# Kernel tuning notes

Hardware: AMD Instinct MI355X
Metric: run time of the kernel (lower is better)

The kernel has to match this reference:

```python
import jax, jax.numpy as jnp
import numpy as np
from jax import lax

H, W = 32, 32
HEADS = 8
EPS_LN = 1e-5


def layer_norm(x, g, b):
    mu = jnp.mean(x, axis=-1, keepdims=True)
    var = jnp.mean((x - mu) ** 2, axis=-1, keepdims=True)
    return (x - mu) * lax.rsqrt(var + EPS_LN) * g + b


def l2norm(x):  # F.normalize along last dim, eps=1e-12
    n = jnp.sqrt(jnp.sum(x * x, axis=-1, keepdims=True))
    return x / jnp.maximum(n, 1e-12)


def channel_attention(x, qkv_w, temp, proj_w, proj_b):
    B, N, C = x.shape
    d = C // HEADS
    qkv = (x @ qkv_w).reshape(B, N, 3, HEADS, d).transpose(2, 0, 3, 1, 4)  # [3,B,h,N,d]
    q, k, v = qkv[0], qkv[1], qkv[2]
    q = l2norm(q.swapaxes(-2, -1))  # [B,h,d,N], normalized over N
    k = l2norm(k.swapaxes(-2, -1))
    v = v.swapaxes(-2, -1)          # [B,h,d,N]
    attn = jnp.einsum('bhdn,bhen->bhde', q, k) * temp  # [B,h,d,d]
    attn = jax.nn.softmax(attn, axis=-1)
    out = jnp.einsum('bhde,bhen->bhdn', attn, v)       # [B,h,d,N]
    out = out.transpose(0, 3, 1, 2).reshape(B, N, C)
    return out @ proj_w + proj_b


def cross_attention(x1, x2, rp_w, rp_b, cn_g, cn_b):
    # head_count = 1 (efficient/linear attention)
    B, N, D = x1.shape
    keys = x2.swapaxes(1, 2)            # [B,D,N]
    values = x1.swapaxes(1, 2)          # [B,D,N]
    key = jax.nn.softmax(keys, axis=2)  # softmax over tokens
    query = jax.nn.softmax(keys, axis=1)  # softmax over channels
    context = jnp.einsum('bdn,ben->bde', key, values)     # [B,Dk,Dv]
    attended = jnp.einsum('bde,bdn->ben', context, query)  # [B,Dv,N]
    agg = attended.reshape(B, D, H, W)
    # 1x1 conv reprojection D -> 2D
    rep = jnp.einsum('bdhw,ed->behw', agg, rp_w) + rp_b[None, :, None, None]
    rep = rep.reshape(B, 2 * D, N).transpose(0, 2, 1)     # [B,N,2D]
    return layer_norm(rep, cn_g, cn_b)


def mix_ffn(x, fc1_w, fc1_b, dw_w, dw_b, fc2_w, fc2_b):
    B, N, _ = x.shape
    c2 = fc1_w.shape[1]
    h1 = x @ fc1_w + fc1_b                                 # [B,N,c2]
    t = h1.swapaxes(1, 2).reshape(B, c2, H, W)
    conv = lax.conv_general_dilated(
        t, dw_w, window_strides=(1, 1), padding='SAME',
        feature_group_count=c2,
        dimension_numbers=('NCHW', 'OIHW', 'NCHW')) + dw_b[None, :, None, None]
    h2 = conv.reshape(B, c2, N).swapaxes(1, 2)             # [B,N,c2]
    return jax.nn.gelu(h2, approximate=False) @ fc2_w + fc2_b


def reference(x1, x2, ln1_g, ln1_b, ca_qkv_w, ca_temp, ca_proj_w, ca_proj_b,
              ln3_g, ln3_b, rp_w, rp_b, cn_g, cn_b, ln2_g, ln2_b,
              fc1_w, fc1_b, dw_w, dw_b, fc2_w, fc2_b):
    # NOTE: original code uses norm1 + channel_attn1 on BOTH streams
    channel1 = x1 + channel_attention(layer_norm(x1, ln1_g, ln1_b), ca_qkv_w, ca_temp, ca_proj_w, ca_proj_b)
    channel2 = x2 + channel_attention(layer_norm(x2, ln1_g, ln1_b), ca_qkv_w, ca_temp, ca_proj_w, ca_proj_b)
    n1 = layer_norm(channel1, ln3_g, ln3_b)
    n2 = layer_norm(channel2, ln3_g, ln3_b)
    attn = cross_attention(n1, n2, rp_w, rp_b, cn_g, cn_b)
    tx = jnp.concatenate([channel1, channel2], axis=2) + attn  # [B,N,2D]
    mx = tx + mix_ffn(layer_norm(tx, ln2_g, ln2_b), fc1_w, fc1_b, dw_w, dw_b, fc2_w, fc2_b)
    return mx


def setup_inputs() -> dict:
    key = jax.random.key(0)
    ks = jax.random.split(key, 8)
    B, N, D = 16, 1024, 384
    s = 0.02
    return {
        'x1': jax.random.normal(ks[0], (B, N, D), jnp.float32),
        'x2': jax.random.normal(ks[1], (B, N, D), jnp.float32),
        'ln1_g': jnp.ones((D,), jnp.float32), 'ln1_b': jnp.zeros((D,), jnp.float32),
        'ca_qkv_w': jax.random.normal(ks[2], (D, 3 * D), jnp.float32) * s,
        'ca_temp': jnp.ones((HEADS, 1, 1), jnp.float32),
        'ca_proj_w': jax.random.normal(ks[3], (D, D), jnp.float32) * s,
        'ca_proj_b': jnp.zeros((D,), jnp.float32),
        'ln3_g': jnp.ones((D,), jnp.float32), 'ln3_b': jnp.zeros((D,), jnp.float32),
        'rp_w': jax.random.normal(ks[4], (2 * D, D), jnp.float32) * s,
        'rp_b': jnp.zeros((2 * D,), jnp.float32),
        'cn_g': jnp.ones((2 * D,), jnp.float32), 'cn_b': jnp.zeros((2 * D,), jnp.float32),
        'ln2_g': jnp.ones((2 * D,), jnp.float32), 'ln2_b': jnp.zeros((2 * D,), jnp.float32),
        'fc1_w': jax.random.normal(ks[5], (2 * D, 4 * D), jnp.float32) * s,
        'fc1_b': jnp.zeros((4 * D,), jnp.float32),
        'dw_w': jax.random.normal(ks[6], (4 * D, 1, 3, 3), jnp.float32) * s,
        'dw_b': jnp.zeros((4 * D,), jnp.float32),
        'fc2_w': jax.random.normal(ks[7], (4 * D, 2 * D), jnp.float32) * s,
        'fc2_b': jnp.zeros((2 * D,), jnp.float32),
    }
```

## Files before the change

### kernel.cpp

```cpp
#include <hip/hip_runtime.h>
#include <math.h>

#define BN 16
#define NN 1024
#define DD 384
#define D2 768
#define C2 1536
#define NHEAD 8
#define DH 48

#define SZ_ND   (BN*NN*DD)
#define SZ_N2D  (BN*NN*D2)
#define SZ_NC2  (BN*NN*C2)
#define M2      32768
#define MH      16384

typedef __bf16 bf16x8 __attribute__((ext_vector_type(8)));
typedef float f32x4v __attribute__((ext_vector_type(4)));
typedef unsigned short u16x4 __attribute__((ext_vector_type(4)));

__device__ __forceinline__ unsigned short f2bf(float x){
  unsigned int u = __float_as_uint(x);
  u += 0x7FFFu + ((u >> 16) & 1u);
  return (unsigned short)(u >> 16);
}
__device__ __forceinline__ float bf2f(unsigned short h){
  return __uint_as_float(((unsigned int)h) << 16);
}

__device__ __forceinline__ float blockReduceSum256(float v){
  __shared__ float red[4];
  #pragma unroll
  for (int o=32;o;o>>=1) v += __shfl_down(v,o,64);
  if ((threadIdx.x&63)==0) red[threadIdx.x>>6]=v;
  __syncthreads();
  float r = red[0]+red[1]+red[2]+red[3];
  __syncthreads();
  return r;
}
__device__ __forceinline__ float blockReduceMax256(float v){
  __shared__ float red[4];
  #pragma unroll
  for (int o=32;o;o>>=1) v = fmaxf(v, __shfl_down(v,o,64));
  if ((threadIdx.x&63)==0) red[threadIdx.x>>6]=v;
  __syncthreads();
  float r = fmaxf(fmaxf(red[0],red[1]),fmaxf(red[2],red[3]));
  __syncthreads();
  return r;
}

__global__ __launch_bounds__(256) void ln_kernel(const float* __restrict__ in,
    const float* __restrict__ g, const float* __restrict__ b,
    float* __restrict__ out, int C){
  const int row = blockIdx.x;
  const float* x = in + (size_t)row*C;
  float s=0.f;
  for (int i=threadIdx.x;i<C;i+=256) s += x[i];
  s = blockReduceSum256(s);
  const float mu = s / (float)C;
  float v=0.f;
  for (int i=threadIdx.x;i<C;i+=256){ float d = x[i]-mu; v += d*d; }
  v = blockReduceSum256(v);
  const float rs = rsqrtf(v/(float)C + 1e-5f);
  float* o = out + (size_t)row*C;
  for (int i=threadIdx.x;i<C;i+=256) o[i] = (x[i]-mu)*rs*g[i] + b[i];
}

__global__ __launch_bounds__(256) void ln_split2_kernel(const float* __restrict__ in1,
    const float* __restrict__ in2, int Mh,
    const float* __restrict__ g, const float* __restrict__ b,
    unsigned short* __restrict__ oh, unsigned short* __restrict__ ol, int C){
  const int row = blockIdx.x;
  const float* x = (row < Mh) ? (in1 + (size_t)row*C) : (in2 + (size_t)(row-Mh)*C);
  float s=0.f;
  for (int i=threadIdx.x;i<C;i+=256) s += x[i];
  s = blockReduceSum256(s);
  const float mu = s / (float)C;
  float v=0.f;
  for (int i=threadIdx.x;i<C;i+=256){ float d = x[i]-mu; v += d*d; }
  v = blockReduceSum256(v);
  const float rs = rsqrtf(v/(float)C + 1e-5f);
  unsigned short* ohp = oh + (size_t)row*C;
  unsigned short* olp = ol + (size_t)row*C;
  for (int i=threadIdx.x;i<C;i+=256){
    float val = (x[i]-mu)*rs*g[i] + b[i];
    unsigned short hh = f2bf(val);
    ohp[i] = hh; olp[i] = f2bf(val - bf2f(hh));
  }
}

__global__ __launch_bounds__(256) void rowsoftmax_split_kernel(const float* __restrict__ in,
    unsigned short* __restrict__ oh, unsigned short* __restrict__ ol, int C){
  const int row = blockIdx.x;
  const float* x = in + (size_t)row*C;
  float m = -3.0e38f;
  for (int i=threadIdx.x;i<C;i+=256) m = fmaxf(m, x[i]);
  m = blockReduceMax256(m);
  float s = 0.f;
  for (int i=threadIdx.x;i<C;i+=256) s += expf(x[i]-m);
  s = blockReduceSum256(s);
  const float inv = 1.f/s;
  unsigned short* ohp = oh + (size_t)row*C;
  unsigned short* olp = ol + (size_t)row*C;
  for (int i=threadIdx.x;i<C;i+=256){
    float p = expf(x[i]-m)*inv;
    unsigned short hh = f2bf(p);
    ohp[i] = hh; olp[i] = f2bf(p - bf2f(hh));
  }
}

__global__ __launch_bounds__(256) void colsoftmax_tsplit_kernel(const float* __restrict__ in,
    unsigned short* __restrict__ oh, unsigned short* __restrict__ ol){
  __shared__ float tile[64][33];
  __shared__ unsigned short outh[32][66], outl[32][66];
  __shared__ float redm[8][32], reds[8][32];
  const int d0 = blockIdx.x*32, b = blockIdx.y;
  const int t = threadIdx.x, dl = t & 31, nc = t >> 5;
  const float* p = in + (size_t)b*NN*DD + d0;

  float m_run = -3.0e38f, s_run = 0.f;
  for (int tb = 0; tb < 16; tb++){
    const int n0 = tb*64;
    #pragma unroll
    for (int k=0;k<8;k++){
      int e = t + k*256;
      int row = e >> 5, col = e & 31;
      tile[row][col] = p[(size_t)(n0+row)*DD + col];
    }
    __syncthreads();
    float lm = -3.0e38f;
    #pragma unroll
    for (int r=0;r<8;r++) lm = fmaxf(lm, tile[nc*8+r][dl]);
    redm[nc][dl] = lm;
    __syncthreads();
    float tm = redm[0][dl];
    #pragma unroll
    for (int q=1;q<8;q++) tm = fmaxf(tm, redm[q][dl]);
    float m_new = fmaxf(m_run, tm);
    float ls = 0.f;
    #pragma unroll
    for (int r=0;r<8;r++) ls += expf(tile[nc*8+r][dl] - m_new);
    reds[nc][dl] = ls;
    __syncthreads();
    float ts = reds[0][dl];
    #pragma unroll
    for (int q=1;q<8;q++) ts += reds[q][dl];
    s_run = s_run * expf(m_run - m_new) + ts;
    m_run = m_new;
    __syncthreads();
  }

  const float inv = 1.f / s_run, mm = m_run;
  unsigned short* qh = oh + ((size_t)b*DD + d0)*NN;
  unsigned short* ql = ol + ((size_t)b*DD + d0)*NN;
  for (int tb = 0; tb < 16; tb++){
    const int n0 = tb*64;
    #pragma unroll
    for (int k=0;k<8;k++){
      int e = t + k*256;
      int row = e >> 5, col = e & 31;
      tile[row][col] = p[(size_t)(n0+row)*DD + col];
    }
    __syncthreads();
    #pragma unroll
    for (int r=0;r<8;r++){
      int row = nc*8 + r;
      float val = expf(tile[row][dl] - mm) * inv;
      unsigned short hh = f2bf(val);
      outh[dl][row] = hh;
      outl[dl][row] = f2bf(val - bf2f(hh));
    }
    __syncthreads();
    #pragma unroll
    for (int k=0;k<8;k++){
      int e = t + k*256;
      int dd = e >> 6, nn = e & 63;
      qh[(size_t)dd*NN + n0 + nn] = outh[dd][nn];
      ql[(size_t)dd*NN + n0 + nn] = outl[dd][nn];
    }
    __syncthreads();
  }
}

__global__ __launch_bounds__(256) void tsplit_kernel(const float* __restrict__ in,
    unsigned short* __restrict__ oh, unsigned short* __restrict__ ol, int R, int Cc){
  const size_t zb = (size_t)blockIdx.z * R * Cc;
  const float* ip = in + zb;
  unsigned short* ohp = oh + zb;
  unsigned short* olp = ol + zb;
  __shared__ float tile[32][33];
  const int c0 = blockIdx.x*32, r0 = blockIdx.y*32;
  const int j = threadIdx.x & 31, i4 = threadIdx.x >> 5;
  #pragma unroll
  for (int s=0;s<4;s++){
    int i = i4*4+s;
    tile[i][j] = ip[(size_t)(r0+i)*Cc + c0 + j];
  }
  __syncthreads();
  #pragma unroll
  for (int s=0;s<4;s++){
    int i = i4*4+s;
    float x = tile[j][i];
    unsigned short h = f2bf(x);
    ohp[(size_t)(c0+i)*R + r0 + j] = h;
    olp[(size_t)(c0+i)*R + r0 + j] = f2bf(x - bf2f(h));
  }
}

__global__ __launch_bounds__(256) void chattn_mfma_kernel(
    const unsigned int* __restrict__ qp, const float* __restrict__ temp,
    unsigned short* __restrict__ coh, unsigned short* __restrict__ col)
{
  const int bh = blockIdx.x, b = bh >> 3, h = bh & 7;
  const int t = threadIdx.x, w = t >> 6, lane = t & 63;
  const int lr = lane & 15, g = lane >> 4;

  __shared__ __align__(16) unsigned char ldsA[27648];
  unsigned short (*Qh)[72] = (unsigned short(*)[72])(ldsA);
  unsigned short (*Ql)[72] = (unsigned short(*)[72])(ldsA + 6912);
  unsigned short (*Kh)[72] = (unsigned short(*)[72])(ldsA + 13824);
  unsigned short (*Kl)[72] = (unsigned short(*)[72])(ldsA + 20736);
  unsigned short (*Vh)[72] = (unsigned short(*)[72])(ldsA);
  unsigned short (*Vl)[72] = (unsigned short(*)[72])(ldsA + 9216);
  __shared__ unsigned short Ph[48][72], Pl[48][72];
  __shared__ float S[48][49];
  __shared__ float qn[48], kn[48];

  const size_t base = (size_t)b*NN*1152 + (size_t)h*48;

  int agrp[3], apr[3], aoff[3];
  #pragma unroll
  for (int l=0;l<3;l++){
    int idx = l*256+t;
    int mo = (idx>=384) ? 1 : 0;
    int a = idx - mo*384;
    agrp[l] = a%12; apr[l] = a/12; aoff[l] = mo*384;
  }

  f32x4v acc[12];
  #pragma unroll
  for (int i=0;i<12;i++) acc[i] = (f32x4v){0.f,0.f,0.f,0.f};

  uint4 p0[3], p1[3];
  #pragma unroll
  for (int l=0;l<3;l++){
    const size_t a = base + (size_t)(apr[l]*2)*1152 + aoff[l] + agrp[l]*4;
    p0[l] = *(const uint4*)(qp + a);
    p1[l] = *(const uint4*)(qp + a + 1152);
  }

  for (int nc=0; nc<16; nc++){
    #pragma unroll
    for (int l=0;l<3;l++){
      unsigned short (*Dh)[72] = aoff[l] ? Kh : Qh;
      unsigned short (*Dl)[72] = aoff[l] ? Kl : Ql;
      const unsigned w0[4] = {p0[l].x, p0[l].y, p0[l].z, p0[l].w};
      const unsigned w1[4] = {p1[l].x, p1[l].y, p1[l].z, p1[l].w};
      #pragma unroll
      for (int c=0;c<4;c++){
        int d = agrp[l]*4+c;
        *(unsigned int*)&Dh[d][apr[l]*2] = (w0[c] & 0xffffu) | (w1[c] << 16);
        *(unsigned int*)&Dl[d][apr[l]*2] = (w0[c] >> 16)     | (w1[c] & 0xffff0000u);
      }
    }
    __syncthreads();
    if (nc < 15){
      #pragma unroll
      for (int l=0;l<3;l++){
        const size_t a = base + (size_t)((nc+1)*64 + apr[l]*2)*1152 + aoff[l] + agrp[l]*4;
        p0[l] = *(const uint4*)(qp + a);
        p1[l] = *(const uint4*)(qp + a + 1152);
      }
    }
    if (w < 3){
      #pragma unroll
      for (int ks=0;ks<2;ks++){
        bf16x8 a_h = *(const bf16x8*)&Qh[w*16+lr][ks*32+g*8];
        bf16x8 a_l = *(const bf16x8*)&Ql[w*16+lr][ks*32+g*8];
        #pragma unroll
        for (int c=0;c<3;c++){
          bf16x8 b_h = *(const bf16x8*)&Kh[c*16+lr][ks*32+g*8];
          bf16x8 b_l = *(const bf16x8*)&Kl[c*16+lr][ks*32+g*8];
          acc[c] = __builtin_amdgcn_mfma_f32_16x16x32_bf16(a_h, b_h, acc[c], 0,0,0);
          acc[c] = __builtin_amdgcn_mfma_f32_16x16x32_bf16(a_l, b_h, acc[c], 0,0,0);
          acc[c] = __builtin_amdgcn_mfma_f32_16x16x32_bf16(a_h, b_l, acc[c], 0,0,0);
        }
      }
    } else {
      #pragma unroll
      for (int ks=0;ks<2;ks++){
        #pragma unroll
        for (int c=0;c<3;c++){
          bf16x8 qh_ = *(const bf16x8*)&Qh[c*16+lr][ks*32+g*8];
          bf16x8 ql_ = *(const bf16x8*)&Ql[c*16+lr][ks*32+g*8];
          bf16x8 kh_ = *(const bf16x8*)&Kh[c*16+lr][ks*32+g*8];
          bf16x8 kl_ = *(const bf16x8*)&Kl[c*16+lr][ks*32+g*8];
          acc[c]   = __builtin_amdgcn_mfma_f32_16x16x32_bf16(qh_, qh_, acc[c],   0,0,0);
          acc[3+c] = __builtin_amdgcn_mfma_f32_16x16x32_bf16(qh_, ql_, acc[3+c], 0,0,0);
          acc[6+c] = __builtin_amdgcn_mfma_f32_16x16x32_bf16(kh_, kh_, acc[6+c], 0,0,0);
          acc[9+c] = __builtin_amdgcn_mfma_f32_16x16x32_bf16(kh_, kl_, acc[9+c], 0,0,0);
        }
      }
    }
    __syncthreads();
  }

  const float tp = temp[h];
  if (w == 3){
    if ((lane>>4) == ((lane&15)>>2)){
      int p = lane & 15, r = p & 3;
      #pragma unroll
      for (int c=0;c<3;c++){
        float q2 = fmaxf(acc[c][r]   + 2.f*acc[3+c][r], 0.f);
        float k2 = fmaxf(acc[6+c][r] + 2.f*acc[9+c][r], 0.f);
        qn[c*16+p] = fmaxf(sqrtf(q2), 1e-12f);
        kn[c*16+p] = fmaxf(sqrtf(k2), 1e-12f);
      }
    }
  }
  __syncthreads();
  if (w < 3){
    #pragma unroll
    for (int c=0;c<3;c++){
      #pragma unroll
      for (int r=0;r<4;r++){
        int i = w*16 + g*4 + r, j = c*16 + lr;
        S[i][j] = acc[c][r]*tp/(qn[i]*kn[j]);
      }
    }
  }
  __syncthreads();

  int vgrp[3], vtk[3];
  #pragma unroll
  for (int l=0;l<3;l++){ int idx=l*256+t; vtk[l]=idx/12; vgrp[l]=idx%12; }
  uint4 pv[3];
  #pragma unroll
  for (int l=0;l<3;l++){
    const size_t a = base + (size_t)vtk[l]*1152 + 768 + vgrp[l]*4;
    pv[l] = *(const uint4*)(qp + a);
  }

  if (t < 48){
    float m = -3.0e38f;
    for (int j=0;j<48;j++) m = fmaxf(m, S[t][j]);
    float s = 0.f;
    for (int j=0;j<48;j++){ float e_ = expf(S[t][j]-m); S[t][j] = e_; s += e_; }
    float inv = 1.f/s;
    for (int j=0;j<48;j++){
      float p = S[t][j]*inv;
      unsigned short hp = f2bf(p);
      Ph[t][j] = hp; Pl[t][j] = f2bf(p - bf2f(hp));
    }
    #pragma unroll
    for (int j=48;j<64;j++){ Ph[t][j]=0; Pl[t][j]=0; }
  } else {
    const u16x4 z4 = (u16x4){0,0,0,0};
    for (int idx=t-48; idx<512; idx+=208){
      int tk = idx>>3, q = idx&7;
      if (q<4) *(u16x4*)&Vh[tk][48+(q&3)*4] = z4;
      else     *(u16x4*)&Vl[tk][48+(q&3)*4] = z4;
    }
  }
  __syncthreads();

  bf16x8 pfh[3][2], pfl[3][2];
  #pragma unroll
  for (int it=0;it<3;it++)
    #pragma unroll
    for (int ks=0;ks<2;ks++){
      pfh[it][ks] = *(const bf16x8*)&Ph[it*16+lr][ks*32+g*8];
      pfl[it][ks] = *(const bf16x8*)&Pl[it*16+lr][ks*32+g*8];
    }

  for (int vc=0; vc<16; vc++){
    #pragma unroll
    for (int l=0;l<3;l++){
      const unsigned pw[4] = {pv[l].x, pv[l].y, pv[l].z, pv[l].w};
      u16x4 hv, lv;
      #pragma unroll
      for (int c=0;c<4;c++){
        hv[c] = (unsigned short)(pw[c] & 0xffffu);
        lv[c] = (unsigned short)(pw[c] >> 16);
      }
      *(u16x4*)&Vh[vtk[l]][vgrp[l]*4] = hv;
      *(u16x4*)&Vl[vtk[l]][vgrp[l]*4] = lv;
    }
    __syncthreads();
    if (vc < 15){
      #pragma unroll
      for (int l=0;l<3;l++){
        const size_t a = base + (size_t)((vc+1)*64+vtk[l])*1152 + 768 + vgrp[l]*4;
        pv[l] = *(const uint4*)(qp + a);
      }
    }
    bf16x8 vfh[2], vfl[2];
    #pragma unroll
    for (int ks=0;ks<2;ks++){
      vfh[ks] = *(const bf16x8*)&Vh[w*16+lr][ks*32+g*8];
      vfl[ks] = *(const bf16x8*)&Vl[w*16+lr][ks*32+g*8];
    }
    f32x4v o[3];
    #pragma unroll
    for (int it=0;it<3;it++) o[it] = (f32x4v){0.f,0.f,0.f,0.f};
    #pragma unroll
    for (int it=0;it<3;it++)
      #pragma unroll
      for (int ks=0;ks<2;ks++){
        o[it] = __builtin_amdgcn_mfma_f32_16x16x32_bf16(pfh[it][ks], vfh[ks], o[it], 0,0,0);
        o[it] = __builtin_amdgcn_mfma_f32_16x16x32_bf16(pfl[it][ks], vfh[ks], o[it], 0,0,0);
        o[it] = __builtin_amdgcn_mfma_f32_16x16x32_bf16(pfh[it][ks], vfl[ks], o[it], 0,0,0);
      }
    const int n = vc*64 + w*16 + lr;
    #pragma unroll
    for (int it=0;it<3;it++){
      const size_t off = ((size_t)b*NN + n)*DD + h*48 + it*16 + g*4;
      u16x4 hv, lv;
      #pragma unroll
      for (int r=0;r<4;r++){
        float x = o[it][r];
        unsigned short hh = f2bf(x);
        hv[r] = hh; lv[r] = f2bf(x - bf2f(hh));
      }
      *(u16x4*)(coh + off) = hv;
      *(u16x4*)(col + off) = lv;
    }
    __syncthreads();
  }
}

__global__ __launch_bounds__(256) void wprep2_kernel(
    const float* __restrict__ qkvw, unsigned short* __restrict__ qwh, unsigned short* __restrict__ qwl,
    const float* __restrict__ projw, unsigned short* __restrict__ pwh, unsigned short* __restrict__ pwl)
{
  __shared__ float tile[32][33];
  const int bid = blockIdx.x;
  const float* in; unsigned short *oh, *ol; int Nin, bx, by;
  if (bid < 432){ in = qkvw;  oh = qwh; ol = qwl; Nin = 1152; bx = bid % 36; by = bid / 36; }
  else { int k = bid - 432; in = projw; oh = pwh; ol = pwl; Nin = DD;   bx = k % 12;  by = k / 12; }
  const int n0 = bx*32, k0 = by*32;
  const int j = threadIdx.x & 31, i4 = threadIdx.x >> 5;
  #pragma unroll
  for (int s=0;s<4;s++){
    int i = i4*4+s;
    tile[i][j] = in[(size_t)(k0+i)*Nin + n0 + j];
  }
  __syncthreads();
  #pragma unroll
  for (int s=0;s<4;s++){
    int i = i4*4+s;
    float x = tile[j][i];
    unsigned short h = f2bf(x);
    oh[(size_t)(n0+i)*DD + k0 + j] = h;
    ol[(size_t)(n0+i)*DD + k0 + j] = f2bf(x - bf2f(h));
  }
}

__global__ __launch_bounds__(256) void wconv_t_kernel(const float* __restrict__ in,
    unsigned short* __restrict__ oh, unsigned short* __restrict__ ol, int K, int Nin){
  __shared__ float tile[32][33];
  const int n0 = blockIdx.x*32, k0 = blockIdx.y*32;
  const int j = threadIdx.x & 31, i4 = threadIdx.x >> 5;
  #pragma unroll
  for (int s=0;s<4;s++){
    int i = i4*4+s;
    tile[i][j] = (n0 + j < Nin) ? in[(size_t)(k0+i)*Nin + n0 + j] : 0.f;
  }
  __syncthreads();
  #pragma unroll
  for (int s=0;s<4;s++){
    int i = i4*4+s;
    float x = tile[j][i];
    unsigned short h = f2bf(x);
    oh[(size_t)(n0+i)*K + k0 + j] = h;
    ol[(size_t)(n0+i)*K + k0 + j] = f2bf(x - bf2f(h));
  }
}

__global__ __launch_bounds__(256) void wconv_kernel(const float* __restrict__ in,
    unsigned short* __restrict__ oh, unsigned short* __restrict__ ol, int n){
  int i = blockIdx.x*256 + threadIdx.x;
  if (i < n){
    float x = in[i];
    unsigned short h = f2bf(x);
    oh[i] = h;
    ol[i] = f2bf(x - bf2f(h));
  }
}

template<bool BIAS_, bool RES_, bool SPLIT_, bool PACK32_>
__global__ __launch_bounds__(256) void gemm_bf16x3s_kernel(
    const unsigned short* __restrict__ Ah, const unsigned short* __restrict__ Al,
    const unsigned short* __restrict__ Bh, const unsigned short* __restrict__ Bl,
    const float* __restrict__ bias, const float* __restrict__ res,
    const float* __restrict__ res2, int Mh2,
    float* __restrict__ C, unsigned short* __restrict__ Ch, unsigned short* __restrict__ Cl,
    int M, int N, int K, size_t sAz, size_t sBz, size_t sCz)
{
  const int t = threadIdx.x;
  const int nwg = gridDim.x*gridDim.y;
  const int lin = blockIdx.y*gridDim.x + blockIdx.x;
  const int swz = ((nwg & 7)==0) ? ((lin & 7)*(nwg >> 3) + (lin >> 3)) : lin;
  const int bx = swz % gridDim.x, by = swz / gridDim.x;
  const int m0 = by*128, n0 = bx*128;
  const size_t zo = (size_t)blockIdx.z;

  __shared__ unsigned short As_h0[128][32], As_l0[128][32];
  __shared__ unsigned short Bs_h0[128][32], Bs_l0[128][32];
  __shared__ unsigned short As_h1[128][32], As_l1[128][32];
  __shared__ unsigned short Bs_h1[128][32], Bs_l1[128][32];

  const unsigned short* Ahb = Ah + zo*sAz + (size_t)m0*K;
  const unsigned short* Alb = Al + zo*sAz + (size_t)m0*K;
  const unsigned short* Bhb = Bh + zo*sBz + (size_t)n0*K;
  const unsigned short* Blb = Bl + zo*sBz + (size_t)n0*K;

  f32x4v acc[4][4];
  #pragma unroll
  for (int i=0;i<4;i++)
    #pragma unroll
    for (int j=0;j<4;j++) acc[i][j] = (f32x4v){0.f,0.f,0.f,0.f};

  const int w  = t >> 6;
  const int wm = w >> 1, wn = w & 1;
  const int lr = t & 15, g = (t & 63) >> 4;
  const int srow = t >> 1;
  const int kb0  = (t & 1)*2;
  const int ssw  = (srow >> 1) & 3;
  const int ks0  = ((kb0+0) ^ ssw)*8;
  const int ks1  = ((kb0+1) ^ ssw)*8;

  uint4 aAh0,aAh1,aAl0,aAl1,aBh0,aBh1,aBl0,aBl1;
  uint4 bAh0,bAh1,bAl0,bAl1,bBh0,bBh1,bBl0,bBl1;

#define LOADT(P, K0) { \
    const size_t go0 = (size_t)srow*K + (size_t)(K0) + (size_t)(kb0*8); \
    P##Ah0 = *(const uint4*)(Ahb + go0); P##Ah1 = *(const uint4*)(Ahb + go0 + 8); \
    P##Al0 = *(const uint4*)(Alb + go0); P##Al1 = *(const uint4*)(Alb + go0 + 8); \
    P##Bh0 = *(const uint4*)(Bhb + go0); P##Bh1 = *(const uint4*)(Bhb + go0 + 8); \
    P##Bl0 = *(const uint4*)(Blb + go0); P##Bl1 = *(const uint4*)(Blb + go0 + 8); }

#define WRITET(BUF, P) { \
    *(uint4*)&As_h##BUF[srow][ks0] = P##Ah0; *(uint4*)&As_h##BUF[srow][ks1] = P##Ah1; \
    *(uint4*)&As_l##BUF[srow][ks0] = P##Al0; *(uint4*)&As_l##BUF[srow][ks1] = P##Al1; \
    *(uint4*)&Bs_h##BUF[srow][ks0] = P##Bh0; *(uint4*)&Bs_h##BUF[srow][ks1] = P##Bh1; \
    *(uint4*)&Bs_l##BUF[srow][ks0] = P##Bl0; *(uint4*)&Bs_l##BUF[srow][ks1] = P##Bl1; }

#define COMPUTET(BUF) { \
    bf16x8 ah[4], al[4], bhf[4], blf[4]; \
    _Pragma("unroll") \
    for (int i=0;i<4;i++){ \
      const int ra = wm*64 + i*16 + lr; \
      const int ka = (g ^ ((ra>>1)&3))*8; \
      ah[i]  = *(const bf16x8*)&As_h##BUF[ra][ka]; \
      al[i]  = *(const bf16x8*)&As_l##BUF[ra][ka]; \
      const int rb = wn*64 + i*16 + lr; \
      const int kb = (g ^ ((rb>>1)&3))*8; \
      bhf[i] = *(const bf16x8*)&Bs_h##BUF[rb][kb]; \
      blf[i] = *(const bf16x8*)&Bs_l##BUF[rb][kb]; \
    } \
    _Pragma("unroll") \
    for (int mi=0;mi<4;mi++) \
      _Pragma("unroll") \
      for (int ni=0;ni<4;ni++){ \
        f32x4v c_ = acc[mi][ni]; \
        c_ = __builtin_amdgcn_mfma_f32_16x16x32_bf16(ah[mi], bhf[ni], c_, 0,0,0); \
        c_ = __builtin_amdgcn_mfma_f32_16x16x32_bf16(al[mi], bhf[ni], c_, 0,0,0); \
        c_ = __builtin_amdgcn_mfma_f32_16x16x32_bf16(ah[mi], blf[ni], c_, 0,0,0); \
        acc[mi][ni] = c_; \
      } }

  const int nk = K >> 5;
  LOADT(a, 0);
  WRITET(0, a);
  LOADT(a, 32);
  __syncthreads();

  for (int kt = 0; kt < nk; kt += 2){
    if (kt+2 < nk) LOADT(b, (kt+2)*32);
    COMPUTET(0);
    WRITET(1, a);
    __syncthreads();
    if (kt+3 < nk) LOADT(a, (kt+3)*32);
    COMPUTET(1);
    if (kt+2 < nk){ WRITET(0, b); }
    __syncthreads();
  }

#undef LOADT
#undef WRITET
#undef COMPUTET

  if (PACK32_){
    unsigned int* Cp = (unsigned int*)Ch + zo*sCz;
    #pragma unroll
    for (int ni=0;ni<4;ni++){
      const int col = n0 + wn*64 + ni*16 + lr;
      #pragma unroll
      for (int mi=0;mi<4;mi++){
        const int r0 = m0 + wm*64 + mi*16 + g*4;
        #pragma unroll
        for (int r=0;r<4;r++){
          float v = acc[mi][ni][r];
          unsigned short hv = f2bf(v);
          unsigned short lv = f2bf(v - bf2f(hv));
          Cp[(size_t)(r0+r)*N + col] = (unsigned)hv | ((unsigned)lv << 16);
        }
      }
    }
  } else if (SPLIT_){
    unsigned short* Chb = Ch + zo*sCz;
    unsigned short* Clb = Cl + zo*sCz;
    #pragma unroll
    for (int ni=0;ni<4;ni++){
      const int col = n0 + wn*64 + ni*16 + lr;
      #pragma unroll
      for (int mi=0;mi<4;mi++){
        const int r0 = m0 + wm*64 + mi*16 + g*4;
        #pragma unroll
        for (int r=0;r<4;r++){
          float v = acc[mi][ni][r];
          unsigned short hv = f2bf(v);
          const size_t off = (size_t)(r0+r)*N + col;
          Chb[off] = hv;
          Clb[off] = f2bf(v - bf2f(hv));
        }
      }
    }
  } else {
    float* Cb = C + zo*sCz;
    const float* resb = nullptr;
    size_t roff = 0;
    if (RES_){
      if (res2 != nullptr && m0 >= Mh2){ resb = res2; roff = (size_t)Mh2; }
      else resb = res + zo*sCz;
    }
    #pragma unroll
    for (int ni=0;ni<4;ni++){
      const int col = n0 + wn*64 + ni*16 + lr;
      const float bb = BIAS_ ? bias[col] : 0.f;
      #pragma unroll
      for (int mi=0;mi<4;mi++){
        const int r0 = m0 + wm*64 + mi*16 + g*4;
        #pragma unroll
        for (int r=0;r<4;r++){
          float v = acc[mi][ni][r] + bb;
          if (RES_) v += resb[((size_t)(r0+r) - roff)*N + col];
          Cb[(size_t)(r0+r)*N + col] = v;
        }
      }
    }
  }
}

__global__ __launch_bounds__(256) void ln_concat_ln2_kernel(const float* __restrict__ rep,
    const float* __restrict__ g1, const float* __restrict__ b1,
    const float* __restrict__ ch1, const float* __restrict__ ch2,
    const float* __restrict__ g2, const float* __restrict__ b2,
    float* __restrict__ tx, unsigned short* __restrict__ y2h, unsigned short* __restrict__ y2l){
  const int row = blockIdx.x;
  const float* x = rep + (size_t)row*D2;
  float xv[3];
  float s=0.f;
  #pragma unroll
  for (int q=0;q<3;q++){ xv[q] = x[threadIdx.x + q*256]; s += xv[q]; }
  s = blockReduceSum256(s);
  const float mu = s / (float)D2;
  float v=0.f;
  #pragma unroll
  for (int q=0;q<3;q++){ float d = xv[q]-mu; v += d*d; }
  v = blockReduceSum256(v);
  const float rs = rsqrtf(v/(float)D2 + 1e-5f);
  float tv[3];
  #pragma unroll
  for (int q=0;q<3;q++){
    int i = threadIdx.x + q*256;
    float val = (xv[q]-mu)*rs*g1[i] + b1[i];
    float rv = (i<DD) ? ch1[(size_t)row*DD + i] : ch2[(size_t)row*DD + i - DD];
    tv[q] = val + rv;
    tx[(size_t)row*D2 + i] = tv[q];
  }
  float s2 = tv[0]+tv[1]+tv[2];
  s2 = blockReduceSum256(s2);
  const float mu2 = s2 / (float)D2;
  float v2=0.f;
  #pragma unroll
  for (int q=0;q<3;q++){ float d = tv[q]-mu2; v2 += d*d; }
  v2 = blockReduceSum256(v2);
  const float rs2 = rsqrtf(v2/(float)D2 + 1e-5f);
  #pragma unroll
  for (int q=0;q<3;q++){
    int i = threadIdx.x + q*256;
    float y = (tv[q]-mu2)*rs2*g2[i] + b2[i];
    unsigned short hh = f2bf(y);
    y2h[(size_t)row*D2 + i] = hh;
    y2l[(size_t)row*D2 + i] = f2bf(y - bf2f(hh));
  }
}

__global__ __launch_bounds__(256) void dwconv_gelu_kernel(const float* __restrict__ h1,
    const float* __restrict__ w, const float* __restrict__ bias,
    unsigned short* __restrict__ gh, unsigned short* __restrict__ gl){
  const int idx = blockIdx.x*256 + threadIdx.x;
  const int b   = idx / 12288;
  const int r   = idx - b*12288;
  const int hh  = r / 384;
  const int c4  = r - hh*384;
  const int c   = c4*4;
  const float* base = h1 + (size_t)b*NN*C2 + c;
  const size_t obase = ((size_t)b*NN + hh*32)*C2 + c;

  f32x4v wk[9];
  #pragma unroll
  for (int k=0;k<9;k++){
    f32x4v t_;
    #pragma unroll
    for (int q=0;q<4;q++) t_[q] = w[(size_t)(c+q)*9 + k];
    wk[k] = t_;
  }
  f32x4v bvv;
  {
    const float4 bb = *(const float4*)(bias + c);
    bvv = (f32x4v){bb.x, bb.y, bb.z, bb.w};
  }

  const bool hm = (hh > 0), hp = (hh < 31);
  const f32x4v z4 = (f32x4v){0.f,0.f,0.f,0.f};
  const size_t rm = (size_t)((hh-1)*32)*C2;
  const size_t r0 = (size_t)( hh   *32)*C2;
  const size_t rp = (size_t)((hh+1)*32)*C2;

  f32x4v A0,A1,A2, B0,B1,B2, C0,C1,C2c;
  A0=z4; A1=z4; A2=z4;
  B0 = hm ? *(const f32x4v*)(base + rm) : z4;
  B1 =      *(const f32x4v*)(base + r0);
  B2 = hp ? *(const f32x4v*)(base + rp) : z4;
  C0 = hm ? *(const f32x4v*)(base + rm + C2) : z4;
  C1 =      *(const f32x4v*)(base + r0 + C2);
  C2c= hp ? *(const f32x4v*)(base + rp + C2) : z4;

  for (int ww=0; ww<32; ww++){
    f32x4v N0,N1,N2;
    if (ww < 30){
      const size_t co_ = (size_t)(ww+2)*C2;
      N0 = hm ? *(const f32x4v*)(base + rm + co_) : z4;
      N1 =      *(const f32x4v*)(base + r0 + co_) ;
      N2 = hp ? *(const f32x4v*)(base + rp + co_) : z4;
    } else { N0=z4; N1=z4; N2=z4; }

    f32x4v s = bvv;
    s += wk[0]*A0 + wk[1]*B0 + wk[2]*C0;
    s += wk[3]*A1 + wk[4]*B1 + wk[5]*C1;
    s += wk[6]*A2 + wk[7]*B2 + wk[8]*C2c;

    u16x4 hv, lv;
    #pragma unroll
    for (int q=0;q<4;q++){
      float rlt = 0.5f*s[q]*(1.f + erff(s[q]*0.70710678118654752f));
      unsigned short hhv = f2bf(rlt);
      hv[q] = hhv; lv[q] = f2bf(rlt - bf2f(hhv));
    }
    *(u16x4*)(gh + obase + (size_t)ww*C2) = hv;
    *(u16x4*)(gl + obase + (size_t)ww*C2) = lv;

    A0=B0; A1=B1; A2=B2;
    B0=C0; B1=C1; B2=C2c;
    C0=N0; C1=N1; C2c=N2;
  }
}

extern "C" void kernel_launch(void* const* d_in, const int* in_sizes, int n_in,
                              void* d_out, int out_size, void* d_ws, size_t ws_size,
                              hipStream_t stream) {
  const float* x1     = (const float*)d_in[0];
  const float* x2     = (const float*)d_in[1];
  const float* ln1_g  = (const float*)d_in[2];
  const float* ln1_b  = (const float*)d_in[3];
  const float* qkv_w  = (const float*)d_in[4];
  const float* ca_temp= (const float*)d_in[5];
  const float* proj_w = (const float*)d_in[6];
  const float* proj_b = (const float*)d_in[7];
  const float* ln3_g  = (const float*)d_in[8];
  const float* ln3_b  = (const float*)d_in[9];
  const float* rp_w   = (const float*)d_in[10];
  const float* rp_b   = (const float*)d_in[11];
  const float* cn_g   = (const float*)d_in[12];
  const float* cn_b   = (const float*)d_in[13];
  const float* ln2_g  = (const float*)d_in[14];
  const float* ln2_b  = (const float*)d_in[15];
  const float* fc1_w  = (const float*)d_in[16];
  const float* fc1_b  = (const float*)d_in[17];
  const float* dw_w   = (const float*)d_in[18];
  const float* dw_b   = (const float*)d_in[19];
  const float* fc2_w  = (const float*)d_in[20];
  const float* fc2_b  = (const float*)d_in[21];
  float* out = (float*)d_out;
  float* W   = (float*)d_ws;

  unsigned short* ycoh = (unsigned short*)out;
  unsigned short* ycol = ycoh + 12582912u;
  unsigned short* coh  = ycoh;
  unsigned short* col  = ycol;
  unsigned int*   qkvp = (unsigned int*)W;
  unsigned short* qkvwT_h  = (unsigned short*)(W + 37748736ull);
  unsigned short* qkvwT_l  = qkvwT_h + 442368u;
  unsigned short* projwT_h = qkvwT_l + 442368u;
  unsigned short* projwT_l = projwT_h + 147456u;
  float* ch12 = W;
  float* n12  = W + 12582912ull;
  unsigned short* QSh = (unsigned short*)(W + 25165824ull);
  unsigned short* QSl = QSh + 6291456u;
  unsigned short* KSt_h = (unsigned short*)(W + 31457280ull);
  unsigned short* KSt_l = KSt_h + 6291456u;
  unsigned short* rpw_h = (unsigned short*)(W + 37748736ull);
  unsigned short* rpw_l = rpw_h + 294912u;
  unsigned short* n1t_h = (unsigned short*)(W + 38043648ull);
  unsigned short* n1t_l = n1t_h + 6291456u;
  unsigned short* ctxT_h = (unsigned short*)(W + 12582912ull);
  unsigned short* ctxT_l = ctxT_h + 2359296u;
  unsigned short* ATbh = (unsigned short*)(W + 14942208ull);
  unsigned short* ATbl = ATbh + 6291456u;
  float* rep = W + 25165824ull;
  float* txp = out;
  unsigned short* y2h = (unsigned short*)(W + 37748736ull);
  unsigned short* y2l = y2h + 12582912u;
  float* h1 = W;
  unsigned short* fc1wT_h = (unsigned short*)(W + 25165824ull);
  unsigned short* fc1wT_l = fc1wT_h + 1179648u;
  unsigned short* gh = (unsigned short*)(W + 25165824ull);
  unsigned short* gl = (unsigned short*)(W + 37748736ull);
  unsigned short* fc2wT_h = (unsigned short*)W;
  unsigned short* fc2wT_l = fc2wT_h + 1179648u;

  wprep2_kernel<<<dim3(576), dim3(256), 0, stream>>>(
      qkv_w, qkvwT_h, qkvwT_l, proj_w, projwT_h, projwT_l);

  ln_split2_kernel<<<dim3(M2), dim3(256), 0, stream>>>(x1, x2, MH, ln1_g, ln1_b, ycoh, ycol, DD);
  gemm_bf16x3s_kernel<false,false,false,true><<<dim3(1152/128, M2/128), dim3(256), 0, stream>>>(
      ycoh, ycol, qkvwT_h, qkvwT_l, nullptr, nullptr, nullptr, 0,
      nullptr, (unsigned short*)qkvp, nullptr, M2, 1152, DD, 0,0,0);
  chattn_mfma_kernel<<<dim3(32*NHEAD), dim3(256), 0, stream>>>(qkvp, ca_temp, coh, col);
  gemm_bf16x3s_kernel<true,true,false,false><<<dim3(DD/128, M2/128), dim3(256), 0, stream>>>(
      coh, col, projwT_h, projwT_l, proj_b, x1, x2, MH,
      ch12, nullptr, nullptr, M2, DD, DD, 0,0,0);

  wconv_kernel<<<dim3(294912/256), dim3(256), 0, stream>>>(rp_w, rpw_h, rpw_l, 294912);
  ln_kernel<<<dim3(M2), dim3(256), 0, stream>>>(ch12, ln3_g, ln3_b, n12, DD);
  const float* n2half = n12 + (size_t)MH*DD;
  rowsoftmax_split_kernel<<<dim3(MH), dim3(256), 0, stream>>>(n2half, QSh, QSl, DD);
  colsoftmax_tsplit_kernel<<<dim3(DD/32, BN), dim3(256), 0, stream>>>(n2half, KSt_h, KSt_l);
  tsplit_kernel<<<dim3(DD/32, NN/32, BN), dim3(256), 0, stream>>>(n12, n1t_h, n1t_l, NN, DD);
  gemm_bf16x3s_kernel<false,false,true,false><<<dim3(DD/128, DD/128, BN), dim3(256), 0, stream>>>(
      n1t_h, n1t_l, KSt_h, KSt_l, nullptr, nullptr, nullptr, 0,
      nullptr, ctxT_h, ctxT_l, DD, DD, NN, (size_t)DD*NN, (size_t)DD*NN, (size_t)DD*DD);
  gemm_bf16x3s_kernel<false,false,true,false><<<dim3(DD/128, NN/128, BN), dim3(256), 0, stream>>>(
      QSh, QSl, ctxT_h, ctxT_l, nullptr, nullptr, nullptr, 0,
      nullptr, ATbh, ATbl, NN, DD, DD, (size_t)NN*DD, (size_t)DD*DD, (size_t)NN*DD);
  gemm_bf16x3s_kernel<true,false,false,false><<<dim3(D2/128, MH/128), dim3(256), 0, stream>>>(
      ATbh, ATbl, rpw_h, rpw_l, rp_b, nullptr, nullptr, 0,
      rep, nullptr, nullptr, MH, D2, DD, 0,0,0);
  ln_concat_ln2_kernel<<<dim3(MH), dim3(256), 0, stream>>>(
      rep, cn_g, cn_b, ch12, ch12 + (size_t)MH*DD, ln2_g, ln2_b, txp, y2h, y2l);

  wconv_t_kernel<<<dim3(C2/32, D2/32), dim3(256), 0, stream>>>(fc1_w, fc1wT_h, fc1wT_l, D2, C2);
  gemm_bf16x3s_kernel<true,false,false,false><<<dim3(C2/128, MH/128), dim3(256), 0, stream>>>(
      y2h, y2l, fc1wT_h, fc1wT_l, fc1_b, nullptr, nullptr, 0,
      h1, nullptr, nullptr, MH, C2, D2, 0,0,0);
  dwconv_gelu_kernel<<<dim3(196608/256), dim3(256), 0, stream>>>(h1, dw_w, dw_b, gh, gl);
  wconv_t_kernel<<<dim3(D2/32, C2/32), dim3(256), 0, stream>>>(fc2_w, fc2wT_h, fc2wT_l, C2, D2);
  gemm_bf16x3s_kernel<true,true,false,false><<<dim3(D2/128, MH/128), dim3(256), 0, stream>>>(
      gh, gl, fc2wT_h, fc2wT_l, fc2_b, txp, nullptr, 0,
      out, nullptr, nullptr, MH, D2, C2, 0,0,0);
}
```

Baseline: 847.8 us.

## Add 256x256-tile 8-wave bf16x3 GEMM with phased prefetch for FFN and reprojection

```diff
diff --git a/kernel.cpp b/kernel.cpp
--- a/kernel.cpp
+++ b/kernel.cpp
@@ -648,6 +648,130 @@
           if (RES_) v += resb[((size_t)(r0+r) - roff)*N + col];
           Cb[(size_t)(r0+r)*N + col] = v;
         }
+      }
+    }
+  }
+}
+
+template<bool BIAS_, bool RES_>
+__global__ __launch_bounds__(512, 2) void gemm_bf16x3_8ph_kernel(
+    const unsigned short* __restrict__ Ah, const unsigned short* __restrict__ Al,
+    const unsigned short* __restrict__ Bh, const unsigned short* __restrict__ Bl,
+    const float* __restrict__ bias, const float* __restrict__ res,
+    float* __restrict__ C, int M, int N, int K)
+{
+  const int t = threadIdx.x;
+  const int nwg = gridDim.x*gridDim.y;
+  const int lin = blockIdx.y*gridDim.x + blockIdx.x;
+  const int swz = ((nwg & 7)==0) ? ((lin & 7)*(nwg >> 3) + (lin >> 3)) : lin;
+  const int bx = swz % gridDim.x, by = swz / gridDim.x;
+  const int m0 = by*256, n0 = bx*256;
+
+  __shared__ unsigned short As_h[2][256][32], As_l[2][256][32];
+  __shared__ unsigned short Bs_h[2][256][32], Bs_l[2][256][32];
+
+  const unsigned short* Ahb = Ah + (size_t)m0*K;
+  const unsigned short* Alb = Al + (size_t)m0*K;
+  const unsigned short* Bhb = Bh + (size_t)n0*K;
+  const unsigned short* Blb = Bl + (size_t)n0*K;
+
+  f32x4v acc[8][4];
+  #pragma unroll
+  for (int i=0;i<8;i++)
+    #pragma unroll
+    for (int j=0;j<4;j++) acc[i][j] = (f32x4v){0.f,0.f,0.f,0.f};
+
+  const int w  = t >> 6;
+  const int wm = w >> 2, wn = w & 3;
+  const int lr = t & 15, g = (t & 63) >> 4;
+  const int srow = t >> 1;
+  const int kb0  = (t & 1)*2;
+  const int ssw  = (srow >> 1) & 3;
+  const int ks0  = ((kb0+0) ^ ssw)*8;
+  const int ks1  = ((kb0+1) ^ ssw)*8;
+
+  uint4 aA0,aA1,aA2,aA3, aB0,aB1,aB2,aB3;
+  uint4 bA0,bA1,bA2,bA3, bB0,bB1,bB2,bB3;
+  bf16x8 bh_[4], bl_[4];
+
+#define GBAR() { asm volatile("s_waitcnt lgkmcnt(0)" ::: "memory"); \
+                 __builtin_amdgcn_s_barrier(); }
+#define LOAD_A(P, K0) { const size_t go = (size_t)srow*K + (size_t)(K0) + (size_t)(kb0*8); \
+    P##A0 = *(const uint4*)(Ahb+go); P##A1 = *(const uint4*)(Ahb+go+8); \
+    P##A2 = *(const uint4*)(Alb+go); P##A3 = *(const uint4*)(Alb+go+8); }
+#define LOAD_B(P, K0) { const size_t go = (size_t)srow*K + (size_t)(K0) + (size_t)(kb0*8); \
+    P##B0 = *(const uint4*)(Bhb+go); P##B1 = *(const uint4*)(Bhb+go+8); \
+    P##B2 = *(const uint4*)(Blb+go); P##B3 = *(const uint4*)(Blb+go+8); }
+#define WRITET(BUF, P) { \
+    *(uint4*)&As_h[BUF][srow][ks0]=P##A0; *(uint4*)&As_h[BUF][srow][ks1]=P##A1; \
+    *(uint4*)&As_l[BUF][srow][ks0]=P##A2; *(uint4*)&As_l[BUF][srow][ks1]=P##A3; \
+    *(uint4*)&Bs_h[BUF][srow][ks0]=P##B0; *(uint4*)&Bs_h[BUF][srow][ks1]=P##B1; \
+    *(uint4*)&Bs_l[BUF][srow][ks0]=P##B2; *(uint4*)&Bs_l[BUF][srow][ks1]=P##B3; }
+#define READ_B(BUF) { _Pragma("unroll") for (int ni=0;ni<4;ni++){ \
+    const int rb = wn*64 + ni*16 + lr; const int kb = (g ^ ((rb>>1)&3))*8; \
+    bh_[ni] = *(const bf16x8*)&Bs_h[BUF][rb][kb]; \
+    bl_[ni] = *(const bf16x8*)&Bs_l[BUF][rb][kb]; } }
+#define PHASE(BUF, MI, EXTRA) { \
+    bf16x8 ah0_, ah1_, al0_, al1_; \
+    { const int ra0 = wm*128 + (MI)*16 + lr;   const int ka0 = (g ^ ((ra0>>1)&3))*8; \
+      const int ra1 = wm*128 + (MI+1)*16 + lr; const int ka1 = (g ^ ((ra1>>1)&3))*8; \
+      ah0_ = *(const bf16x8*)&As_h[BUF][ra0][ka0]; al0_ = *(const bf16x8*)&As_l[BUF][ra0][ka0]; \
+      ah1_ = *(const bf16x8*)&As_h[BUF][ra1][ka1]; al1_ = *(const bf16x8*)&As_l[BUF][ra1][ka1]; } \
+    EXTRA \
+    GBAR(); \
+    __builtin_amdgcn_s_setprio(1); \
+    _Pragma("unroll") for (int ni=0;ni<4;ni++){ \
+      f32x4v c0 = acc[MI][ni], c1 = acc[MI+1][ni]; \
+      c0 = __builtin_amdgcn_mfma_f32_16x16x32_bf16(ah0_, bh_[ni], c0, 0,0,0); \
+      c0 = __builtin_amdgcn_mfma_f32_16x16x32_bf16(al0_, bh_[ni], c0, 0,0,0); \
+      c0 = __builtin_amdgcn_mfma_f32_16x16x32_bf16(ah0_, bl_[ni], c0, 0,0,0); \
+      c1 = __builtin_amdgcn_mfma_f32_16x16x32_bf16(ah1_, bh_[ni], c1, 0,0,0); \
+      c1 = __builtin_amdgcn_mfma_f32_16x16x32_bf16(al1_, bh_[ni], c1, 0,0,0); \
+      c1 = __builtin_amdgcn_mfma_f32_16x16x32_bf16(ah1_, bl_[ni], c1, 0,0,0); \
+      acc[MI][ni] = c0; acc[MI+1][ni] = c1; } \
+    __builtin_amdgcn_s_setprio(0); \
+    GBAR(); }
+
+  const int nk = K >> 5;
+  LOAD_A(a, 0); LOAD_B(a, 0);
+  WRITET(0, a);
+  LOAD_A(a, 32); LOAD_B(a, 32);
+  __syncthreads();
+
+  for (int kt = 0; kt < nk; kt += 2){
+    const bool pf = (kt+2 < nk);
+    const bool pf3 = (kt+3 < nk);
+    READ_B(0);
+    PHASE(0, 0, ;)
+    PHASE(0, 2, if (pf){ LOAD_A(b, (kt+2)*32); })
+    PHASE(0, 4, if (pf){ LOAD_B(b, (kt+2)*32); })
+    PHASE(0, 6, WRITET(1, a);)
+    READ_B(1);
+    PHASE(1, 0, ;)
+    PHASE(1, 2, if (pf3){ LOAD_A(a, (kt+3)*32); })
+    PHASE(1, 4, if (pf3){ LOAD_B(a, (kt+3)*32); })
+    PHASE(1, 6, if (pf){ WRITET(0, b); })
+  }
+
+#undef GBAR
+#undef LOAD_A
+#undef LOAD_B
+#undef WRITET
+#undef READ_B
+#undef PHASE
+
+  #pragma unroll
+  for (int ni=0;ni<4;ni++){
+    const int col = n0 + wn*64 + ni*16 + lr;
+    const float bb = BIAS_ ? bias[col] : 0.f;
+    #pragma unroll
+    for (int mi=0;mi<8;mi++){
+      const int r0 = m0 + wm*128 + mi*16 + g*4;
+      #pragma unroll
+      for (int r=0;r<4;r++){
+        float v = acc[mi][ni][r] + bb;
+        if (RES_) v += res[(size_t)(r0+r)*N + col];
+        C[(size_t)(r0+r)*N + col] = v;
       }
     }
   }
@@ -856,19 +980,16 @@
   gemm_bf16x3s_kernel<false,false,true,false><<<dim3(DD/128, NN/128, BN), dim3(256), 0, stream>>>(
       QSh, QSl, ctxT_h, ctxT_l, nullptr, nullptr, nullptr, 0,
       nullptr, ATbh, ATbl, NN, DD, DD, (size_t)NN*DD, (size_t)DD*DD, (size_t)NN*DD);
-  gemm_bf16x3s_kernel<true,false,false,false><<<dim3(D2/128, MH/128), dim3(256), 0, stream>>>(
-      ATbh, ATbl, rpw_h, rpw_l, rp_b, nullptr, nullptr, 0,
-      rep, nullptr, nullptr, MH, D2, DD, 0,0,0);
+  gemm_bf16x3_8ph_kernel<true,false><<<dim3(D2/256, MH/256), dim3(512), 0, stream>>>(
+      ATbh, ATbl, rpw_h, rpw_l, rp_b, nullptr, rep, MH, D2, DD);
   ln_concat_ln2_kernel<<<dim3(MH), dim3(256), 0, stream>>>(
       rep, cn_g, cn_b, ch12, ch12 + (size_t)MH*DD, ln2_g, ln2_b, txp, y2h, y2l);
 
   wconv_t_kernel<<<dim3(C2/32, D2/32), dim3(256), 0, stream>>>(fc1_w, fc1wT_h, fc1wT_l, D2, C2);
-  gemm_bf16x3s_kernel<true,false,false,false><<<dim3(C2/128, MH/128), dim3(256), 0, stream>>>(
-      y2h, y2l, fc1wT_h, fc1wT_l, fc1_b, nullptr, nullptr, 0,
-      h1, nullptr, nullptr, MH, C2, D2, 0,0,0);
+  gemm_bf16x3_8ph_kernel<true,false><<<dim3(C2/256, MH/256), dim3(512), 0, stream>>>(
+      y2h, y2l, fc1wT_h, fc1wT_l, fc1_b, nullptr, h1, MH, C2, D2);
   dwconv_gelu_kernel<<<dim3(196608/256), dim3(256), 0, stream>>>(h1, dw_w, dw_b, gh, gl);
   wconv_t_kernel<<<dim3(D2/32, C2/32), dim3(256), 0, stream>>>(fc2_w, fc2wT_h, fc2wT_l, C2, D2);
-  gemm_bf16x3s_kernel<true,true,false,false><<<dim3(D2/128, MH/128), dim3(256), 0, stream>>>(
-      gh, gl, fc2wT_h, fc2wT_l, fc2_b, txp, nullptr, 0,
-      out, nullptr, nullptr, MH, D2, C2, 0,0,0);
-}
+  gemm_bf16x3_8ph_kernel<true,true><<<dim3(D2/256, MH/256), dim3(512), 0, stream>>>(
+      gh, gl, fc2wT_h, fc2wT_l, fc2_b, txp, out, MH, D2, C2);
+}
```

Result: slower. 1.053 ms (+24.2%).
